# Performance work log

Hardware: AMD Instinct MI355X
Metric: run time of the kernel (lower is better)

## Reference

```python
import jax, jax.numpy as jnp
import numpy as np

B, Q, K, M, E, H = 2, 1024, 2048, 1024, 1024, 32
HD = E // H
SCALE = HD ** -0.5


def setup_inputs() -> dict:
    key0 = jax.random.key(0)
    ks = jax.random.split(key0, 12)
    inp = {
        "query": jax.random.normal(ks[0], (B, Q, E), jnp.float32),
        "key": jax.random.normal(ks[1], (B, K, E), jnp.float32),
        "value": jax.random.normal(ks[2], (B, K, E), jnp.float32),
        "memory": jax.random.normal(ks[3], (B, M, E), jnp.float32),
        "Wq": jax.random.normal(ks[4], (E, E), jnp.float32) * 0.02,
        "bq": jnp.zeros((E,), jnp.float32),
        "Wk": jax.random.normal(ks[5], (E, E), jnp.float32) * 0.02,
        "bk": jnp.zeros((E,), jnp.float32),
        "Wv": jax.random.normal(ks[6], (E, E), jnp.float32) * 0.02,
        "bv": jnp.zeros((E,), jnp.float32),
        "Wo": jax.random.normal(ks[7], (E, E), jnp.float32) * 0.02,
        "bo": jnp.zeros((E,), jnp.float32),
    }
    return inp


def _heads(x, W, b):
    # nn.Linear: y = x @ W.T + b, then split into heads -> (B, H, L, HD)
    y = jnp.einsum("ble,fe->blf", x, W) + b
    Bv, L, _ = y.shape
    return y.reshape(Bv, L, H, HD).transpose(0, 2, 1, 3)


def reference(query, key, value, memory, Wq, bq, Wk, bk, Wv, bv, Wo, bo):
    q = _heads(query, Wq, bq)        # (B,H,Q,HD)
    k = _heads(key, Wk, bk)          # (B,H,K,HD)
    v = _heads(value, Wv, bv)        # (B,H,K,HD)
    mk = _heads(memory, Wk, bk)      # (B,H,M,HD)
    mv = _heads(memory, Wv, bv)      # (B,H,M,HD)

    attn_scores = jnp.einsum("bhqd,bhkd->bhqk", q, k) * SCALE
    mem_scores = jnp.einsum("bhqd,bhmd->bhqm", q, mk) * SCALE
    combined = jnp.concatenate([attn_scores, mem_scores], axis=-1)  # (B,H,Q,K+M)
    w = jax.nn.softmax(combined, axis=-1)
    cv = jnp.concatenate([v, mv], axis=2)  # (B,H,K+M,HD)
    out = jnp.einsum("bhqk,bhkd->bhqd", w, cv)
    out = out.transpose(0, 2, 1, 3).reshape(query.shape[0], query.shape[1], E)
    return jnp.einsum("bqe,fe->bqf", out, Wo) + bo
```

## Files before the change

kernel.cpp:

```cpp
#include <hip/hip_runtime.h>


typedef float  f32x4  __attribute__((ext_vector_type(4)));
typedef short  bf16x8 __attribute__((ext_vector_type(8)));
typedef unsigned int   u32;
typedef unsigned short u16;
typedef u32 u32x2 __attribute__((ext_vector_type(2)));
typedef u32 u32x4 __attribute__((ext_vector_type(4)));
typedef u16 u16x4 __attribute__((ext_vector_type(4)));

#define SCALE_  0.17677669529663687f
#define LOG2E_  1.4426950408889634f

#if defined(__has_builtin)
#  if __has_builtin(__builtin_amdgcn_exp2f)
#    define EXP2F(x) __builtin_amdgcn_exp2f(x)
#  endif
#endif
#ifndef EXP2F
#  define EXP2F(x) __builtin_exp2f(x)
#endif

static __device__ __forceinline__ u32 bfpack2(float lo, float hi) {
  u32 a = __builtin_bit_cast(u32, lo) + 0x8000u;
  u32 b = __builtin_bit_cast(u32, hi) + 0x8000u;
  return __builtin_amdgcn_perm(b, a, 0x07060302u);
}
static __device__ __forceinline__ u16 bf16of(float x) {
  return (u16)((__builtin_bit_cast(u32, x) + 0x8000u) >> 16);
}
static __device__ __forceinline__ void gld_lds16(const u16* g, u16* l) {
  __builtin_amdgcn_global_load_lds(
      (const __attribute__((address_space(1))) void*)g,
      (__attribute__((address_space(3))) void*)l, 16, 0, 0);
}

__global__ __launch_bounds__(256)
void prep_kernel(const float* __restrict__ q, const float* __restrict__ k,
                 const float* __restrict__ v, const float* __restrict__ m,
                 const float* __restrict__ wq, const float* __restrict__ wk,
                 const float* __restrict__ wv, const float* __restrict__ wo,
                 u16* qs, u16* ks, u16* vs, u16* ms,
                 u16* wqs, u16* wks, u16* wvs, u16* wos) {
  const int bid = blockIdx.x;
  const float* src; u16* dst; int R, r0;
  if (bid < 32)       { src = q;  dst = qs;  R = 2048; r0 = bid * 64; }
  else if (bid < 96)  { src = k;  dst = ks;  R = 4096; r0 = (bid - 32) * 64; }
  else if (bid < 160) { src = v;  dst = vs;  R = 4096; r0 = (bid - 96) * 64; }
  else if (bid < 192) { src = m;  dst = ms;  R = 2048; r0 = (bid - 160) * 64; }
  else if (bid < 208) { src = wq; dst = wqs; R = 1024; r0 = (bid - 192) * 64; }
  else if (bid < 224) { src = wk; dst = wks; R = 1024; r0 = (bid - 208) * 64; }
  else if (bid < 240) { src = wv; dst = wvs; R = 1024; r0 = (bid - 224) * 64; }
  else                { src = wo; dst = wos; R = 1024; r0 = (bid - 240) * 64; }

  for (int i = 0; i < 32; ++i) {
    const int idx = i * 256 + threadIdx.x;
    const int kt  = idx >> 9;
    const int rem = idx & 511;
    const int row = rem >> 3;
    const int c   = rem & 7;
    const float* s = src + (size_t)(r0 + row) * 1024 + kt * 64 + c * 8;
    f32x4 a = *(const f32x4*)s, b = *(const f32x4*)(s + 4);
    u32x4 p;
    p.x = bfpack2(a.x, a.y); p.y = bfpack2(a.z, a.w);
    p.z = bfpack2(b.x, b.y); p.w = bfpack2(b.z, b.w);
    *(u32x4*)&dst[((size_t)kt * R + r0 + row) * 64 + ((c ^ (row & 7)) << 3)] = p;
  }
}

template <int MT>
static __device__ __forceinline__
void gemm_core(const u16* __restrict__ Abase, size_t row0, int RA,
               const u16* __restrict__ Wsw, int bn,
               u16* As, u16* Bs, f32x4 acc[][4]) {
  constexpr int MI = MT / 32;
  const int tid  = threadIdx.x;
  const int lane = tid & 63;
  const int wave = tid >> 6;
  const int ln   = lane & 15;
  const int quad = lane >> 4;
  const int wm   = wave >> 1;
  const int wn   = wave & 1;

#pragma unroll
  for (int i = 0; i < MI; ++i)
#pragma unroll
    for (int j = 0; j < 4; ++j)
      acc[i][j] = (f32x4){0.f, 0.f, 0.f, 0.f};

  for (int kt = 0; kt < 16; ++kt) {
    const u16* Ag = Abase + ((size_t)kt * RA + row0) * 64;
    const u16* Bg = Wsw + ((size_t)kt * 1024 + bn * 128) * 64;
#pragma unroll
    for (int r = 0; r < MI; ++r) {
      const int ii = wave * MI + r;
      gld_lds16(Ag + ii * 512 + lane * 8, &As[ii * 512]);
    }
#pragma unroll
    for (int r = 0; r < 4; ++r) {
      const int ii = wave * 4 + r;
      gld_lds16(Bg + ii * 512 + lane * 8, &Bs[ii * 512]);
    }
    __syncthreads();

#pragma unroll
    for (int kk = 0; kk < 2; ++kk) {
      bf16x8 af[MI], bfr[4];
#pragma unroll
      for (int mi = 0; mi < MI; ++mi) {
        const int row = wm * (MI * 16) + mi * 16 + ln;
        af[mi] = *(const bf16x8*)&As[row * 64 + (((kk * 4 + quad) ^ (ln & 7)) << 3)];
      }
#pragma unroll
      for (int ni = 0; ni < 4; ++ni) {
        const int row = wn * 64 + ni * 16 + ln;
        bfr[ni] = *(const bf16x8*)&Bs[row * 64 + (((kk * 4 + quad) ^ (ln & 7)) << 3)];
      }
#pragma unroll
      for (int mi = 0; mi < MI; ++mi)
#pragma unroll
        for (int ni = 0; ni < 4; ++ni)
          acc[mi][ni] = __builtin_amdgcn_mfma_f32_16x16x32_bf16(af[mi], bfr[ni], acc[mi][ni], 0, 0, 0);
    }
    __syncthreads();
  }
}

__global__ __launch_bounds__(256)
void proj3_kernel(const u16* __restrict__ query_sw,
                  const u16* __restrict__ key_sw,
                  const u16* __restrict__ value_sw,
                  const u16* __restrict__ mem_sw,
                  const u16* __restrict__ Wq_sw, const float* __restrict__ bq,
                  const u16* __restrict__ Wk_sw, const float* __restrict__ bk,
                  const u16* __restrict__ Wv_sw, const float* __restrict__ bv,
                  u16* qp, u16* kcat, u16* vT) {
  __shared__ u16 SH[16896];
  u16* As = SH;
  u16* Bs = SH + 8192;

  const int tid  = threadIdx.x;
  const int lane = tid & 63;
  const int wave = tid >> 6;
  const int ln   = lane & 15;
  const int quad = lane >> 4;
  const int wm   = wave >> 1;
  const int wn   = wave & 1;
  const int bx = blockIdx.x, bn = blockIdx.y;

  const u16* Abase; size_t row0; int RA, bm, bb, l0;
  const u16* W; const float* bias;

  if (bx < 16) {
    bm = bx; Abase = query_sw; row0 = (size_t)bm * 128; RA = 2048;
    W = Wq_sw; bias = bq; bb = 0; l0 = 0;
  } else {
    const int bxx = (bx < 64) ? (bx - 16) : (bx - 64);
    bm = bxx;
    const int gr0 = bxx * 128;
    bb = gr0 / 3072;
    l0 = gr0 - bb * 3072;
    const u16* seq = (bx < 64) ? key_sw : value_sw;
    if (l0 < 2048) { Abase = seq;    row0 = (size_t)bb * 2048 + l0;          RA = 4096; }
    else           { Abase = mem_sw; row0 = (size_t)bb * 1024 + (l0 - 2048); RA = 2048; }
    if (bx < 64) { W = Wk_sw; bias = bk; }
    else         { W = Wv_sw; bias = bv; }
  }

  f32x4 acc[4][4];
  gemm_core<128>(Abase, row0, RA, W, bn, As, Bs, acc);

  if (bx < 64) {
    u16* C = (bx < 16) ? qp : kcat;
    const float scale = (bx < 16) ? (SCALE_ * LOG2E_) : 1.0f;
#pragma unroll
    for (int ni = 0; ni < 4; ++ni) {
      const int gc = bn * 128 + wn * 64 + ni * 16 + ln;
      const float bval = bias[gc];
#pragma unroll
      for (int mi = 0; mi < 4; ++mi) {
        const int gr = bm * 128 + wm * 64 + mi * 16 + quad * 4;
#pragma unroll
        for (int r = 0; r < 4; ++r)
          C[(size_t)(gr + r) * 1024 + gc] = bf16of((acc[mi][ni][r] + bval) * scale);
      }
    }
  } else {
    u16* T = SH;
#pragma unroll
    for (int ni = 0; ni < 4; ++ni) {
      const int fl = wn * 64 + ni * 16 + ln;
      const float bval = bias[bn * 128 + fl];
#pragma unroll
      for (int mi = 0; mi < 4; ++mi) {
        const int kl = wm * 64 + mi * 16 + quad * 4;
#pragma unroll
        for (int r = 0; r < 4; ++r)
          T[(kl + r) * 132 + fl] = bf16of(acc[mi][ni][r] + bval);
      }
    }
    __syncthreads();
    const int fr = tid >> 1;
    const int ch = tid & 1;
    const int fg = bn * 128 + fr;
    const size_t rowg = ((size_t)bb * 32 + (fg >> 5)) * 32 + (fg & 31);
    u16* dstrow = vT + rowg * 3072 + l0 + ch * 64;
#pragma unroll
    for (int x = 0; x < 16; ++x) {
      u16x4 v;
      v.x = T[(ch * 64 + x +  0) * 132 + fr];
      v.y = T[(ch * 64 + x + 16) * 132 + fr];
      v.z = T[(ch * 64 + x + 32) * 132 + fr];
      v.w = T[(ch * 64 + x + 48) * 132 + fr];
      *(u16x4*)&dstrow[x * 4] = v;
    }
  }
}

__global__ __launch_bounds__(256)
void gemm_out_kernel(const u16* __restrict__ attn_sw,
                     const u16* __restrict__ Wo_sw,
                     const float* __restrict__ bo,
                     float* __restrict__ out) {
  __shared__ u16 As[64 * 64];
  __shared__ u16 Bs[128 * 64];
  const int tid  = threadIdx.x;
  const int lane = tid & 63;
  const int wave = tid >> 6;
  const int ln   = lane & 15;
  const int quad = lane >> 4;
  const int wm   = wave >> 1;
  const int wn   = wave & 1;
  const int bm = blockIdx.x, bn = blockIdx.y;

  f32x4 acc[2][4];
  gemm_core<64>(attn_sw, (size_t)bm * 64, 2048, Wo_sw, bn, As, Bs, acc);

#pragma unroll
  for (int ni = 0; ni < 4; ++ni) {
    const int gc = bn * 128 + wn * 64 + ni * 16 + ln;
    const float bval = bo[gc];
#pragma unroll
    for (int mi = 0; mi < 2; ++mi) {
      const int gr = bm * 64 + wm * 32 + mi * 16 + quad * 4;
#pragma unroll
      for (int r = 0; r < 4; ++r)
        out[(size_t)(gr + r) * 1024 + gc] = acc[mi][ni][r] + bval;
    }
  }
}

__global__ __launch_bounds__(256, 3)
void attn_kernel(const u16* __restrict__ qp,
                 const u16* __restrict__ kcat,
                 const u16* __restrict__ vTp,
                 u16* __restrict__ attn_sw) {
  __shared__ u16 PwAll[4 * 64 * 72];

  const int tid  = threadIdx.x;
  const int lane = tid & 63;
  const int wave = tid >> 6;
  const int ln   = lane & 15;
  const int quad = lane >> 4;
  const int bid  = blockIdx.x;
  const int bh   = bid & 63;
  const int qt   = bid >> 6;
  const int b    = bh >> 5;
  const int h    = bh & 31;
  const int q0   = qt * 64;

  bf16x8 qf[4];
#pragma unroll
  for (int mf = 0; mf < 4; ++mf)
    qf[mf] = *(const bf16x8*)&qp[(size_t)(b * 1024 + q0 + mf * 16 + ln) * 1024 + h * 32 + quad * 8];

  f32x4 acc[4][2], accS[4];
#pragma unroll
  for (int mf = 0; mf < 4; ++mf) {
    accS[mf] = (f32x4){0.f, 0.f, 0.f, 0.f};
#pragma unroll
    for (int df = 0; df < 2; ++df) acc[mf][df] = (f32x4){0.f, 0.f, 0.f, 0.f};
  }
  bf16x8 ones;
#pragma unroll
  for (int i = 0; i < 8; ++i) ones[i] = (short)0x3F80;

  const u16* kbase = kcat + (size_t)(b * 3072) * 1024 + h * 32;
  const u16* vbase = vTp + (size_t)(bh * 32) * 3072;
  u16* Pw = &PwAll[wave * (64 * 72)];

  const u16* kp[4];
  const u16* vp[2];
#pragma unroll
  for (int nf = 0; nf < 4; ++nf)
    kp[nf] = kbase + (size_t)(wave * 768 + nf * 16 + ln) * 1024 + quad * 8;
#pragma unroll
  for (int df = 0; df < 2; ++df)
    vp[df] = vbase + (size_t)(df * 16 + ln) * 3072 + wave * 768 + quad * 8;

  for (int ci = 0; ci < 12; ++ci) {
    bf16x8 kf[4], vf[4];
#pragma unroll
    for (int nf = 0; nf < 4; ++nf)
      kf[nf] = *(const bf16x8*)kp[nf];
#pragma unroll
    for (int kk = 0; kk < 2; ++kk)
#pragma unroll
      for (int df = 0; df < 2; ++df)
        vf[kk * 2 + df] = *(const bf16x8*)(vp[df] + kk * 32);

#pragma unroll
    for (int mf = 0; mf < 4; ++mf) {
      f32x4 s[4];
#pragma unroll
      for (int nf = 0; nf < 4; ++nf)
        s[nf] = __builtin_amdgcn_mfma_f32_16x16x32_bf16(qf[mf], kf[nf],
                                                        (f32x4){0.f, 0.f, 0.f, 0.f}, 0, 0, 0);
#pragma unroll
      for (int r = 0; r < 4; ++r) {
        const float p0 = EXP2F(s[0][r]);
        const float p1 = EXP2F(s[1][r]);
        const float p2 = EXP2F(s[2][r]);
        const float p3 = EXP2F(s[3][r]);
        u32x2 pk;
        pk.x = bfpack2(p0, p1);
        pk.y = bfpack2(p2, p3);
        *(u32x2*)&Pw[(mf * 16 + quad * 4 + r) * 72 + ln * 4] = pk;
      }
    }

#pragma unroll
    for (int kk = 0; kk < 2; ++kk)
#pragma unroll
      for (int mf = 0; mf < 4; ++mf) {
        bf16x8 pf = *(const bf16x8*)&Pw[(mf * 16 + ln) * 72 + kk * 32 + quad * 8];
        accS[mf] = __builtin_amdgcn_mfma_f32_16x16x32_bf16(pf, ones, accS[mf], 0, 0, 0);
#pragma unroll
        for (int df = 0; df < 2; ++df)
          acc[mf][df] = __builtin_amdgcn_mfma_f32_16x16x32_bf16(pf, vf[kk * 2 + df], acc[mf][df], 0, 0, 0);
      }

#pragma unroll
    for (int nf = 0; nf < 4; ++nf) kp[nf] += 64 * 1024;
#pragma unroll
    for (int df = 0; df < 2; ++df) vp[df] += 64;
  }

  __syncthreads();
  f32x4* CA = (f32x4*)PwAll;
  f32x4* CS = (f32x4*)&PwAll[16384];
#pragma unroll
  for (int mf = 0; mf < 4; ++mf) {
#pragma unroll
    for (int df = 0; df < 2; ++df)
      CA[((wave * 4 + mf) * 2 + df) * 64 + lane] = acc[mf][df];
    if (ln == 0) CS[(wave * 4 + mf) * 4 + quad] = accS[mf];
  }
  __syncthreads();

  {
    const int mf = wave;
    const int j = ln & 7, chi = ln >> 3;
    f32x4 l = CS[mf * 4 + quad];
#pragma unroll
    for (int w = 1; w < 4; ++w) l += CS[((w * 4) + mf) * 4 + quad];
    f32x4 inv;
#pragma unroll
    for (int r = 0; r < 4; ++r) inv[r] = 1.0f / l[r];
#pragma unroll
    for (int df = 0; df < 2; ++df) {
      f32x4 t = CA[(mf * 2 + df) * 64 + lane];
#pragma unroll
      for (int w = 1; w < 4; ++w) t += CA[(((w * 4) + mf) * 2 + df) * 64 + lane];
      const int c = (h & 1) * 4 + df * 2 + chi;
#pragma unroll
      for (int r = 0; r < 4; ++r) {
        const int row = b * 1024 + q0 + mf * 16 + quad * 4 + r;
        const int cp  = c ^ ((quad * 4 + r) & 7);
        attn_sw[((size_t)(h >> 1) * 2048 + row) * 64 + cp * 8 + j] = bf16of(t[r] * inv[r]);
      }
    }
  }
}

extern "C" void kernel_launch(void* const* d_in, const int* in_sizes, int n_in,
                              void* d_out, int out_size, void* d_ws, size_t ws_size,
                              hipStream_t stream) {
  (void)in_sizes; (void)n_in; (void)out_size; (void)ws_size;
  const float* query  = (const float*)d_in[0];
  const float* key    = (const float*)d_in[1];
  const float* value  = (const float*)d_in[2];
  const float* memory = (const float*)d_in[3];
  const float* Wq = (const float*)d_in[4];
  const float* bq = (const float*)d_in[5];
  const float* Wk = (const float*)d_in[6];
  const float* bk = (const float*)d_in[7];
  const float* Wv = (const float*)d_in[8];
  const float* bv = (const float*)d_in[9];
  const float* Wo = (const float*)d_in[10];
  const float* bo = (const float*)d_in[11];
  float* out = (float*)d_out;

  char* ws = (char*)d_ws;
  const size_t MB = 1024 * 1024;
  u16* query_sw = (u16*)(ws + 0 * MB);
  u16* key_sw   = (u16*)(ws + 4 * MB);
  u16* value_sw = (u16*)(ws + 12 * MB);
  u16* mem_sw   = (u16*)(ws + 20 * MB);
  u16* Wq_sw    = (u16*)(ws + 24 * MB);
  u16* Wk_sw    = (u16*)(ws + 26 * MB);
  u16* Wv_sw    = (u16*)(ws + 28 * MB);
  u16* Wo_sw    = (u16*)(ws + 30 * MB);
  u16* qp       = (u16*)(ws + 32 * MB);
  u16* kcat     = (u16*)(ws + 36 * MB);
  u16* vT       = (u16*)(ws + 48 * MB);
  u16* attn_sw  = (u16*)(ws + 60 * MB);

  dim3 blk(256);
  prep_kernel<<<dim3(256), blk, 0, stream>>>(query, key, value, memory, Wq, Wk, Wv, Wo,
                                             query_sw, key_sw, value_sw, mem_sw,
                                             Wq_sw, Wk_sw, Wv_sw, Wo_sw);
  proj3_kernel<<<dim3(112, 8), blk, 0, stream>>>(query_sw, key_sw, value_sw, mem_sw,
                                                 Wq_sw, bq, Wk_sw, bk, Wv_sw, bv,
                                                 qp, kcat, vT);
  attn_kernel<<<dim3(1024), blk, 0, stream>>>(qp, kcat, vT, attn_sw);
  gemm_out_kernel<<<dim3(32, 8), blk, 0, stream>>>(attn_sw, Wo_sw, bo, out);
}
```

Measured before the change: 235.5 us.

## Keep attention probabilities in registers via transposed S and K16 MFMA for PV

The attention kernel now computes transposed scores (K as the A operand), so the exp'd probabilities already sit in the register layout needed as the B operand of a 16x16x16 bf16 MFMA. This removes the per-wave LDS round trip for P and the ones-vector MFMA used for row sums, which become scalar adds plus a cross-lane shuffle. The V^T layout written by proj3 is reordered to match, and output stores are staged through LDS for 16-byte writes. The output GEMM tile shrinks to 32 rows to launch twice as many blocks, and several launch bounds are raised to target 4 blocks per CU. The trade-off is twice as many K16 MFMAs for PV, plus added register pressure and extra syncs in the epilogue.

```diff
diff --git a/kernel.cpp b/kernel.cpp
--- a/kernel.cpp
+++ b/kernel.cpp
@@ -3,11 +3,13 @@
 
 typedef float  f32x4  __attribute__((ext_vector_type(4)));
 typedef short  bf16x8 __attribute__((ext_vector_type(8)));
+typedef short  bf16x4 __attribute__((ext_vector_type(4)));
 typedef unsigned int   u32;
 typedef unsigned short u16;
 typedef u32 u32x2 __attribute__((ext_vector_type(2)));
 typedef u32 u32x4 __attribute__((ext_vector_type(4)));
 typedef u16 u16x4 __attribute__((ext_vector_type(4)));
+typedef u16 u16x8 __attribute__((ext_vector_type(8)));
 
 #define SCALE_  0.17677669529663687f
 #define LOG2E_  1.4426950408889634f
@@ -19,6 +21,17 @@
 #endif
 #ifndef EXP2F
 #  define EXP2F(x) __builtin_exp2f(x)
+#endif
+
+#if defined(__has_builtin)
+#  if __has_builtin(__builtin_amdgcn_mfma_f32_16x16x16bf16_1k)
+#    define MFMA16K16(A, B, C) __builtin_amdgcn_mfma_f32_16x16x16bf16_1k(A, B, C, 0, 0, 0)
+#  elif __has_builtin(__builtin_amdgcn_mfma_f32_16x16x16_bf16)
+#    define MFMA16K16(A, B, C) __builtin_amdgcn_mfma_f32_16x16x16_bf16(A, B, C, 0, 0, 0)
+#  endif
+#endif
+#ifndef MFMA16K16
+#  define MFMA16K16(A, B, C) __builtin_amdgcn_mfma_f32_16x16x16bf16_1k(A, B, C, 0, 0, 0)
 #endif
 
 static __device__ __forceinline__ u32 bfpack2(float lo, float hi) {
@@ -126,7 +139,7 @@
   }
 }
 
-__global__ __launch_bounds__(256)
+__global__ __launch_bounds__(256, 4)
 void proj3_kernel(const u16* __restrict__ query_sw,
                   const u16* __restrict__ key_sw,
                   const u16* __restrict__ value_sw,
@@ -208,54 +221,51 @@
 #pragma unroll
     for (int x = 0; x < 16; ++x) {
       u16x4 v;
-      v.x = T[(ch * 64 + x +  0) * 132 + fr];
-      v.y = T[(ch * 64 + x + 16) * 132 + fr];
-      v.z = T[(ch * 64 + x + 32) * 132 + fr];
-      v.w = T[(ch * 64 + x + 48) * 132 + fr];
+      v.x = T[(ch * 64 + x * 4 + 0) * 132 + fr];
+      v.y = T[(ch * 64 + x * 4 + 1) * 132 + fr];
+      v.z = T[(ch * 64 + x * 4 + 2) * 132 + fr];
+      v.w = T[(ch * 64 + x * 4 + 3) * 132 + fr];
       *(u16x4*)&dstrow[x * 4] = v;
     }
   }
 }
 
-__global__ __launch_bounds__(256)
+__global__ __launch_bounds__(256, 4)
 void gemm_out_kernel(const u16* __restrict__ attn_sw,
                      const u16* __restrict__ Wo_sw,
                      const float* __restrict__ bo,
                      float* __restrict__ out) {
-  __shared__ u16 As[64 * 64];
+  __shared__ u16 As[32 * 64];
   __shared__ u16 Bs[128 * 64];
   const int tid  = threadIdx.x;
   const int lane = tid & 63;
-  const int wave = tid >> 6;
   const int ln   = lane & 15;
   const int quad = lane >> 4;
+  const int wave = tid >> 6;
   const int wm   = wave >> 1;
   const int wn   = wave & 1;
   const int bm = blockIdx.x, bn = blockIdx.y;
 
-  f32x4 acc[2][4];
-  gemm_core<64>(attn_sw, (size_t)bm * 64, 2048, Wo_sw, bn, As, Bs, acc);
+  f32x4 acc[1][4];
+  gemm_core<32>(attn_sw, (size_t)bm * 32, 2048, Wo_sw, bn, As, Bs, acc);
 
 #pragma unroll
   for (int ni = 0; ni < 4; ++ni) {
     const int gc = bn * 128 + wn * 64 + ni * 16 + ln;
     const float bval = bo[gc];
-#pragma unroll
-    for (int mi = 0; mi < 2; ++mi) {
-      const int gr = bm * 64 + wm * 32 + mi * 16 + quad * 4;
-#pragma unroll
-      for (int r = 0; r < 4; ++r)
-        out[(size_t)(gr + r) * 1024 + gc] = acc[mi][ni][r] + bval;
-    }
-  }
-}
-
-__global__ __launch_bounds__(256, 3)
+    const int gr = bm * 32 + wm * 16 + quad * 4;
+#pragma unroll
+    for (int r = 0; r < 4; ++r)
+      out[(size_t)(gr + r) * 1024 + gc] = acc[0][ni][r] + bval;
+  }
+}
+
+__global__ __launch_bounds__(256, 4)
 void attn_kernel(const u16* __restrict__ qp,
                  const u16* __restrict__ kcat,
                  const u16* __restrict__ vTp,
                  u16* __restrict__ attn_sw) {
-  __shared__ u16 PwAll[4 * 64 * 72];
+  __shared__ u16 SH[18432];
 
   const int tid  = threadIdx.x;
   const int lane = tid & 63;
@@ -274,112 +284,120 @@
   for (int mf = 0; mf < 4; ++mf)
     qf[mf] = *(const bf16x8*)&qp[(size_t)(b * 1024 + q0 + mf * 16 + ln) * 1024 + h * 32 + quad * 8];
 
-  f32x4 acc[4][2], accS[4];
+  f32x4 accT[2][4];
+  float rs[4];
 #pragma unroll
   for (int mf = 0; mf < 4; ++mf) {
-    accS[mf] = (f32x4){0.f, 0.f, 0.f, 0.f};
-#pragma unroll
-    for (int df = 0; df < 2; ++df) acc[mf][df] = (f32x4){0.f, 0.f, 0.f, 0.f};
-  }
-  bf16x8 ones;
-#pragma unroll
-  for (int i = 0; i < 8; ++i) ones[i] = (short)0x3F80;
+    rs[mf] = 0.f;
+#pragma unroll
+    for (int df = 0; df < 2; ++df) accT[df][mf] = (f32x4){0.f, 0.f, 0.f, 0.f};
+  }
 
   const u16* kbase = kcat + (size_t)(b * 3072) * 1024 + h * 32;
   const u16* vbase = vTp + (size_t)(bh * 32) * 3072;
-  u16* Pw = &PwAll[wave * (64 * 72)];
 
   const u16* kp[4];
-  const u16* vp[2];
 #pragma unroll
   for (int nf = 0; nf < 4; ++nf)
     kp[nf] = kbase + (size_t)(wave * 768 + nf * 16 + ln) * 1024 + quad * 8;
+  const u16* vp[2];
 #pragma unroll
   for (int df = 0; df < 2; ++df)
-    vp[df] = vbase + (size_t)(df * 16 + ln) * 3072 + wave * 768 + quad * 8;
+    vp[df] = vbase + (size_t)(df * 16 + ln) * 3072 + wave * 768 + quad * 4;
 
   for (int ci = 0; ci < 12; ++ci) {
-    bf16x8 kf[4], vf[4];
+    bf16x8 kf[4];
 #pragma unroll
     for (int nf = 0; nf < 4; ++nf)
       kf[nf] = *(const bf16x8*)kp[nf];
-#pragma unroll
-    for (int kk = 0; kk < 2; ++kk)
+
+#pragma unroll
+    for (int nf = 0; nf < 4; ++nf) {
+      bf16x4 vf[2];
 #pragma unroll
       for (int df = 0; df < 2; ++df)
-        vf[kk * 2 + df] = *(const bf16x8*)(vp[df] + kk * 32);
-
-#pragma unroll
-    for (int mf = 0; mf < 4; ++mf) {
+        vf[df] = __builtin_bit_cast(bf16x4, *(const u16x4*)(vp[df] + nf * 16));
+
       f32x4 s[4];
 #pragma unroll
-      for (int nf = 0; nf < 4; ++nf)
-        s[nf] = __builtin_amdgcn_mfma_f32_16x16x32_bf16(qf[mf], kf[nf],
+      for (int mf = 0; mf < 4; ++mf)
+        s[mf] = __builtin_amdgcn_mfma_f32_16x16x32_bf16(kf[nf], qf[mf],
                                                         (f32x4){0.f, 0.f, 0.f, 0.f}, 0, 0, 0);
-#pragma unroll
-      for (int r = 0; r < 4; ++r) {
-        const float p0 = EXP2F(s[0][r]);
-        const float p1 = EXP2F(s[1][r]);
-        const float p2 = EXP2F(s[2][r]);
-        const float p3 = EXP2F(s[3][r]);
+
+#pragma unroll
+      for (int mf = 0; mf < 4; ++mf) {
+        const float p0 = EXP2F(s[mf][0]);
+        const float p1 = EXP2F(s[mf][1]);
+        const float p2 = EXP2F(s[mf][2]);
+        const float p3 = EXP2F(s[mf][3]);
+        rs[mf] += (p0 + p1) + (p2 + p3);
         u32x2 pk;
         pk.x = bfpack2(p0, p1);
         pk.y = bfpack2(p2, p3);
-        *(u32x2*)&Pw[(mf * 16 + quad * 4 + r) * 72 + ln * 4] = pk;
+        const bf16x4 pT = __builtin_bit_cast(bf16x4, pk);
+#pragma unroll
+        for (int df = 0; df < 2; ++df)
+          accT[df][mf] = MFMA16K16(vf[df], pT, accT[df][mf]);
       }
     }
 
 #pragma unroll
-    for (int kk = 0; kk < 2; ++kk)
-#pragma unroll
-      for (int mf = 0; mf < 4; ++mf) {
-        bf16x8 pf = *(const bf16x8*)&Pw[(mf * 16 + ln) * 72 + kk * 32 + quad * 8];
-        accS[mf] = __builtin_amdgcn_mfma_f32_16x16x32_bf16(pf, ones, accS[mf], 0, 0, 0);
-#pragma unroll
-        for (int df = 0; df < 2; ++df)
-          acc[mf][df] = __builtin_amdgcn_mfma_f32_16x16x32_bf16(pf, vf[kk * 2 + df], acc[mf][df], 0, 0, 0);
-      }
-
-#pragma unroll
     for (int nf = 0; nf < 4; ++nf) kp[nf] += 64 * 1024;
 #pragma unroll
     for (int df = 0; df < 2; ++df) vp[df] += 64;
   }
 
+  f32x4* CA = (f32x4*)SH;
+  float* CS = (float*)(SH + 16384);
+#pragma unroll
+  for (int mf = 0; mf < 4; ++mf) {
+#pragma unroll
+    for (int df = 0; df < 2; ++df)
+      CA[((wave * 4 + mf) * 2 + df) * 64 + lane] = accT[df][mf];
+    CS[(wave * 4 + mf) * 64 + lane] = rs[mf];
+  }
   __syncthreads();
-  f32x4* CA = (f32x4*)PwAll;
-  f32x4* CS = (f32x4*)&PwAll[16384];
-#pragma unroll
-  for (int mf = 0; mf < 4; ++mf) {
-#pragma unroll
-    for (int df = 0; df < 2; ++df)
-      CA[((wave * 4 + mf) * 2 + df) * 64 + lane] = acc[mf][df];
-    if (ln == 0) CS[(wave * 4 + mf) * 4 + quad] = accS[mf];
-  }
+
+  const int mf = wave;
+  f32x4 t[2];
+  float rsv;
+  {
+    t[0] = CA[((0 * 4 + mf) * 2 + 0) * 64 + lane];
+    t[1] = CA[((0 * 4 + mf) * 2 + 1) * 64 + lane];
+    rsv  = CS[(0 * 4 + mf) * 64 + lane];
+#pragma unroll
+    for (int w = 1; w < 4; ++w) {
+      t[0] += CA[((w * 4 + mf) * 2 + 0) * 64 + lane];
+      t[1] += CA[((w * 4 + mf) * 2 + 1) * 64 + lane];
+      rsv  += CS[(w * 4 + mf) * 64 + lane];
+    }
+  }
+  rsv += __shfl_xor(rsv, 16);
+  rsv += __shfl_xor(rsv, 32);
+  const float inv = 1.0f / rsv;
+
+  u16 ov[2][4];
+#pragma unroll
+  for (int df = 0; df < 2; ++df)
+#pragma unroll
+    for (int r = 0; r < 4; ++r)
+      ov[df][r] = bf16of(t[df][r] * inv);
+
   __syncthreads();
+#pragma unroll
+  for (int df = 0; df < 2; ++df)
+#pragma unroll
+    for (int r = 0; r < 4; ++r)
+      SH[(mf * 16 + ln) * 40 + df * 16 + quad * 4 + r] = ov[df][r];
+  __syncthreads();
 
   {
-    const int mf = wave;
-    const int j = ln & 7, chi = ln >> 3;
-    f32x4 l = CS[mf * 4 + quad];
-#pragma unroll
-    for (int w = 1; w < 4; ++w) l += CS[((w * 4) + mf) * 4 + quad];
-    f32x4 inv;
-#pragma unroll
-    for (int r = 0; r < 4; ++r) inv[r] = 1.0f / l[r];
-#pragma unroll
-    for (int df = 0; df < 2; ++df) {
-      f32x4 t = CA[(mf * 2 + df) * 64 + lane];
-#pragma unroll
-      for (int w = 1; w < 4; ++w) t += CA[(((w * 4) + mf) * 2 + df) * 64 + lane];
-      const int c = (h & 1) * 4 + df * 2 + chi;
-#pragma unroll
-      for (int r = 0; r < 4; ++r) {
-        const int row = b * 1024 + q0 + mf * 16 + quad * 4 + r;
-        const int cp  = c ^ ((quad * 4 + r) & 7);
-        attn_sw[((size_t)(h >> 1) * 2048 + row) * 64 + cp * 8 + j] = bf16of(t[r] * inv[r]);
-      }
-    }
+    const int q  = tid >> 2;
+    const int g  = tid & 3;
+    const u16x8 val = *(const u16x8*)&SH[q * 40 + g * 8];
+    const int qg = b * 1024 + q0 + q;
+    const int cp = (((h & 1) * 4 + g) ^ (qg & 7));
+    *(u16x8*)&attn_sw[((size_t)(h >> 1) * 2048 + qg) * 64 + cp * 8] = val;
   }
 }
 
@@ -424,5 +442,5 @@
                                                  Wq_sw, bq, Wk_sw, bk, Wv_sw, bv,
                                                  qp, kcat, vT);
   attn_kernel<<<dim3(1024), blk, 0, stream>>>(qp, kcat, vT, attn_sw);
-  gemm_out_kernel<<<dim3(32, 8), blk, 0, stream>>>(attn_sw, Wo_sw, bo, out);
-}
+  gemm_out_kernel<<<dim3(64, 8), blk, 0, stream>>>(attn_sw, Wo_sw, bo, out);
+}
```

Result: slower. 240.4 us (+2.1%).
